# Performance work log

Measured on AMD Instinct MI355X. Metric: run time of the kernel, lower is better.

Reference implementation:

```python
import jax, jax.numpy as jnp
import numpy as np

SCORE_THRESH = 0.5
NMS_THRESH = 0.4
TOP_K = 1000  # fixed pre-NMS candidate budget (jit-safe replacement for boolean masking)
STRIDES = (8, 16, 32)
H, W = 2176, 3840


def _anchor_centers(fh, fw, stride):
    yv, xv = jnp.meshgrid(jnp.arange(fh), jnp.arange(fw), indexing='ij')
    return (jnp.stack([xv, yv], -1).reshape(-1, 2).astype(jnp.float32)) * stride  # [N,2]


def _decode_level(scores, bbox, kps, stride):
    fh, fw = H // stride, W // stride
    c = _anchor_centers(fh, fw, stride)                 # [N,2]
    s = jax.nn.sigmoid(scores.reshape(-1))              # [N]
    d = bbox.reshape(-1, 4) * stride                    # [N,4]
    boxes = jnp.concatenate([c - d[:, :2], c + d[:, 2:4]], axis=1)  # x1y1x2y2
    k = kps.reshape(-1, 5, 2) * stride + c[:, None, :]  # (x,y) pairs
    return s, boxes, k.reshape(-1, 10)


def _iou_matrix(b):
    area = (b[:, 2] - b[:, 0]) * (b[:, 3] - b[:, 1])
    lt = jnp.maximum(b[:, None, :2], b[None, :, :2])
    rb = jnp.minimum(b[:, None, 2:], b[None, :, 2:])
    wh = jnp.clip(rb - lt, 0.0)
    inter = wh[..., 0] * wh[..., 1]
    return inter / jnp.clip(area[:, None] + area[None, :] - inter, 1e-9)


def _nms_keep(iou, valid):
    n = iou.shape[0]
    ar = jnp.arange(n)

    def body(i, keep):
        sup = (iou[i] > NMS_THRESH) & (ar > i) & keep[i]
        return keep & ~sup

    return jax.lax.fori_loop(0, n, body, valid)


def reference(x, scores8, bbox8, kps8, scores16, bbox16, kps16, scores32, bbox32, kps32):
    levels = ((scores8, bbox8, kps8), (scores16, bbox16, kps16), (scores32, bbox32, kps32))
    ss, bs, ks = [], [], []
    for (s, b, k), stride in zip(levels, STRIDES):
        si, bi, ki = _decode_level(s, b, k, stride)
        ss.append(si); bs.append(bi); ks.append(ki)
    scores = jnp.concatenate(ss)   # [N_total]
    boxes = jnp.concatenate(bs)    # [N_total,4]
    kpss = jnp.concatenate(ks)     # [N_total,10]

    masked = jnp.where(scores > SCORE_THRESH, scores, -1.0)
    top_s, idx = jax.lax.top_k(masked, TOP_K)
    valid = top_s > SCORE_THRESH
    b = boxes[idx]
    k = kpss[idx]

    keep = jax.lax.stop_gradient(_nms_keep(_iou_matrix(b), valid))
    final_boxes = jnp.where(keep[:, None], b, 0.0)
    final_scores = jnp.where(keep, top_s, 0.0)
    final_kpss = jnp.where(keep[:, None], k, 0.0)
    return final_boxes, final_scores, final_kpss


def setup_inputs() -> dict:
    key = jax.random.key(0)
    ks = jax.random.split(key, 10)
    n8 = (H // 8) * (W // 8)
    n16 = (H // 16) * (W // 16)
    n32 = (H // 32) * (W // 32)
    return {
        'x': jax.random.normal(ks[0], (1, 3, H, W), jnp.float32),
        'scores8': jax.random.normal(ks[1], (1, n8, 1), jnp.float32),
        'bbox8': jax.random.uniform(ks[2], (1, n8, 4), jnp.float32),
        'kps8': jax.random.normal(ks[3], (1, n8, 10), jnp.float32),
        'scores16': jax.random.normal(ks[4], (1, n16, 1), jnp.float32),
        'bbox16': jax.random.uniform(ks[5], (1, n16, 4), jnp.float32),
        'kps16': jax.random.normal(ks[6], (1, n16, 10), jnp.float32),
        'scores32': jax.random.normal(ks[7], (1, n32, 1), jnp.float32),
        'bbox32': jax.random.uniform(ks[8], (1, n32, 4), jnp.float32),
        'kps32': jax.random.normal(ks[9], (1, n32, 10), jnp.float32),
    }
```

## Files before the change

kernel.cpp:

```cpp
#include <hip/hip_runtime.h>
#include <stdint.h>

typedef unsigned int u32;
typedef unsigned long long u64;

#define N8   130560
#define N16  32640
#define N32  8160
#define NTOT 171360
#define NTOT4 42840
#define TOPK 1000
#define NWORDS 16
#define NBINS 512
#define BUCKET_SCALE 85.25f
#define LIST_CAP 2016
#define CPB 32
#define HIST_BLKS 84
#define HIST_THR 512
#define CMP_BLKS 168
#define RANK_BLKS 63
#define IOU_BLKS 63
#define IOU_TASKS (TOPK * NWORDS)
#define NMS_CACHE 256


#define MI_CNT 0
#define MI_IOU 128
#define META_U32 256

#define OFF_PART 0
#define OFF_META 86016
#define OFF_NZ   87040
#define OFF_LIST 87168
#define OFF_MASK 103296

__device__ __forceinline__ u64 ald64(const u64* p) {
  return __hip_atomic_load(p, __ATOMIC_RELAXED, __HIP_MEMORY_SCOPE_AGENT);
}
__device__ __forceinline__ void ast64(u64* p, u64 v) {
  __hip_atomic_store(p, v, __ATOMIC_RELAXED, __HIP_MEMORY_SCOPE_AGENT);
}

__device__ __forceinline__ u32 bucket_of(float x) {
  u32 b = (u32)(x * BUCKET_SCALE);
  return b > (NBINS - 1) ? (NBINS - 1) : b;
}

__device__ __forceinline__ float4 load_logit4(int v, const float* s8, const float* s16,
                                              const float* s32) {
  int e = v * 4;
  if (e < N8) return ((const float4*)s8)[v];
  if (e < N8 + N16) return ((const float4*)s16)[v - N8 / 4];
  return ((const float4*)s32)[v - (N8 + N16) / 4];
}

__device__ __forceinline__ bool iou_gt04(float4 a, float4 b) {
#pragma clang fp contract(off)
  float areaA = (a.z - a.x) * (a.w - a.y);
  float areaB = (b.z - b.x) * (b.w - b.y);
  float ltx = fmaxf(a.x, b.x);
  float lty = fmaxf(a.y, b.y);
  float rbx = fminf(a.z, b.z);
  float rby = fminf(a.w, b.w);
  float wx = rbx - ltx; wx = wx > 0.0f ? wx : 0.0f;
  float wy = rby - lty; wy = wy > 0.0f ? wy : 0.0f;
  float inter = wx * wy;
  float un = areaA + areaB - inter;
  un = un > 1e-9f ? un : 1e-9f;
  return (inter / un) > 0.4f;
}

__device__ __forceinline__ u64 valid_word(int w, u32 vcnt) {
  int lo = w * 64;
  if ((int)vcnt >= lo + 64) return ~0ull;
  if ((int)vcnt <= lo) return 0ull;
  return (1ull << (vcnt - (u32)lo)) - 1ull;
}

__global__ void __launch_bounds__(HIST_THR) k1_hist(
    const float* __restrict__ s8, const float* __restrict__ s16, const float* __restrict__ s32,
    u32* __restrict__ part, u32* __restrict__ meta, u64* __restrict__ nz) {
  __shared__ u32 lh[NBINS];
  const int t = threadIdx.x, blk = blockIdx.x;
  if (t < NBINS) lh[t] = 0;
  __syncthreads();
  int v = blk * HIST_THR + t;
  if (v < NTOT4) {
    float4 x = load_logit4(v, s8, s16, s32);
    if (x.x > 0.0f) atomicAdd(&lh[bucket_of(x.x)], 1u);
    if (x.y > 0.0f) atomicAdd(&lh[bucket_of(x.y)], 1u);
    if (x.z > 0.0f) atomicAdd(&lh[bucket_of(x.z)], 1u);
    if (x.w > 0.0f) atomicAdd(&lh[bucket_of(x.w)], 1u);
  }
  __syncthreads();
  if (t < 256)
    part[blk * 256 + t] = lh[2 * t] | (lh[2 * t + 1] << 16);
  if (blk == 0) {
    if (t < META_U32) meta[t] = 0;
    if (t < NWORDS) nz[t] = 0ull;
  }
}

__global__ void __launch_bounds__(256) k4_compact(
    const float* __restrict__ s8, const float* __restrict__ s16, const float* __restrict__ s32,
    const u32* __restrict__ part, u32* __restrict__ meta, u64* __restrict__ list) {
  __shared__ u32 csum[256];
  __shared__ u32 sB, sBase;
  __shared__ u32 cnt16[16];
  const int t = threadIdx.x, blk = blockIdx.x;
  const int wave = t >> 6, lane = t & 63;
  const int v = blk * 256 + t;
  float4 x = make_float4(-1.f, -1.f, -1.f, -1.f);
  if (v < NTOT4) x = load_logit4(v, s8, s16, s32);

  u32 lo = 0, hi = 0;
  {
    int p = 0;
    for (; p + 4 <= HIST_BLKS; p += 4) {
      u32 a0 = part[(p + 0) * 256 + t];
      u32 a1 = part[(p + 1) * 256 + t];
      u32 a2 = part[(p + 2) * 256 + t];
      u32 a3 = part[(p + 3) * 256 + t];
      lo += (a0 & 0xFFFFu) + (a1 & 0xFFFFu) + (a2 & 0xFFFFu) + (a3 & 0xFFFFu);
      hi += (a0 >> 16) + (a1 >> 16) + (a2 >> 16) + (a3 >> 16);
    }
    for (; p < HIST_BLKS; ++p) {
      u32 a = part[p * 256 + t];
      lo += a & 0xFFFFu; hi += a >> 16;
    }
  }
  csum[t] = lo + hi;
  __syncthreads();
  for (int off = 1; off < 256; off <<= 1) {
    u32 add = (t + off < 256) ? csum[t + off] : 0u;
    __syncthreads();
    csum[t] += add;
    __syncthreads();
  }
  u32 above = (t < 255) ? csum[t + 1] : 0u;
  if (t == 0 && csum[0] < TOPK) sB = 0u;
  if (csum[t] >= TOPK && above < TOPK)
    sB = (above + hi >= TOPK) ? (u32)(2 * t + 1) : (u32)(2 * t);
  __syncthreads();

  const u32 B = sB;
  float c[4] = {x.x, x.y, x.z, x.w};
  u32 win = 0;
#pragma unroll
  for (int j = 0; j < 4; ++j)
    if (c[j] > 0.0f && bucket_of(c[j]) >= B) win |= 1u << j;
  u32 wpos[4], wcnt[4];
#pragma unroll
  for (int j = 0; j < 4; ++j) {
    u64 bal = __ballot((win >> j) & 1u);
    wcnt[j] = (u32)__popcll(bal);
    wpos[j] = (u32)__popcll(bal & ((1ull << lane) - 1ull));
  }
  if (lane == 0) {
#pragma unroll
    for (int j = 0; j < 4; ++j) cnt16[wave * 4 + j] = wcnt[j];
  }
  __syncthreads();
  if (t == 0) {
    u32 tot = 0, pre[16];
#pragma unroll
    for (int k = 0; k < 16; ++k) { pre[k] = tot; tot += cnt16[k]; }
#pragma unroll
    for (int k = 0; k < 16; ++k) cnt16[k] = pre[k];
    sBase = tot ? atomicAdd(&meta[MI_CNT], tot) : 0u;
  }
  __syncthreads();
#pragma unroll
  for (int j = 0; j < 4; ++j) {
    if ((win >> j) & 1u) {
      u32 dst = sBase + cnt16[wave * 4 + j] + wpos[j];
      if (dst < LIST_CAP) {
        u32 idx = (u32)(v * 4 + j);
        list[dst] = ((u64)__float_as_uint(c[j]) << 32) | (u64)(~idx);
      }
    }
  }
}

__global__ void __launch_bounds__(256) k5_rank(
    const u32* __restrict__ meta, const u64* __restrict__ list,
    const float* __restrict__ bb8,  const float* __restrict__ kp8,
    const float* __restrict__ bb16, const float* __restrict__ kp16,
    const float* __restrict__ bb32, const float* __restrict__ kp32,
    float* __restrict__ out) {
  __shared__ __align__(16) u64 keys[LIST_CAP];
  __shared__ u32 rpart[256];
  __shared__ u32 sCnt;
  const int t = threadIdx.x, blk = blockIdx.x;
  if (t == 0) { u32 cc = meta[MI_CNT]; sCnt = cc > LIST_CAP ? LIST_CAP : cc; }
  __syncthreads();
  const u32 cnt = sCnt;
  for (int j = t; j < LIST_CAP; j += 256) keys[j] = (j < (int)cnt) ? list[j] : 0ull;
  __syncthreads();
  {
    const int ci = t & 31, sl = t >> 5;
    const int c = blk * CPB + ci;
    const int chunk = ((int)cnt + 7) >> 3;
    int lo = sl * chunk; if (lo > (int)cnt) lo = (int)cnt;
    int hi = lo + chunk; if (hi > (int)cnt) hi = (int)cnt;
    u64 my = keys[c];
    int r = 0, j = lo;
    for (; j + 4 <= hi; j += 4)
      r += (keys[j] > my) + (keys[j + 1] > my) + (keys[j + 2] > my) + (keys[j + 3] > my);
    for (; j < hi; ++j) r += (keys[j] > my);
    rpart[t] = (u32)r;
  }
  __syncthreads();
  if (t < CPB) {
    const int c = blk * CPB + t;
    if (c < (int)cnt) {
      int rank = 0;
#pragma unroll
      for (int q = 0; q < 8; ++q) rank += (int)rpart[t + 32 * q];
      if (rank < TOPK) {
        u64 my = keys[c];
        float lx = __uint_as_float((u32)(my >> 32));
        float sc = (float)(1.0 / (1.0 + exp(-(double)lx)));
        u32 idx = ~((u32)my);
        float4 box;
        float kv[10];
        int p, xq, yq;
        float st;
        const float *bb, *kp;
        if (idx < N8) {
          st = 8.f;  p = (int)idx;              xq = p % 480; yq = p / 480; bb = bb8;  kp = kp8;
        } else if (idx < N8 + N16) {
          st = 16.f; p = (int)idx - N8;         xq = p % 240; yq = p / 240; bb = bb16; kp = kp16;
        } else {
          st = 32.f; p = (int)idx - (N8 + N16); xq = p % 120; yq = p / 120; bb = bb32; kp = kp32;
        }
        float cx = (float)xq * st, cy = (float)yq * st;
        {
#pragma clang fp contract(off)
          float d0 = bb[4 * p + 0] * st;
          float d1 = bb[4 * p + 1] * st;
          float d2 = bb[4 * p + 2] * st;
          float d3 = bb[4 * p + 3] * st;
          box.x = cx - d0; box.y = cy - d1; box.z = cx + d2; box.w = cy + d3;
          for (int q = 0; q < 10; ++q)
            kv[q] = kp[10 * p + q] * st + ((q & 1) ? cy : cx);
        }
        ((float4*)out)[rank] = box;
        out[4000 + rank] = sc;
#pragma unroll
        for (int q = 0; q < 10; ++q) out[5000 + 10 * rank + q] = kv[q];
      }
    } else if (c < TOPK) {
      ((float4*)out)[c] = make_float4(0.f, 0.f, 0.f, 0.f);
      out[4000 + c] = 0.f;
#pragma unroll
      for (int q = 0; q < 10; ++q) out[5000 + 10 * c + q] = 0.f;
    }
  }
}

__global__ void __launch_bounds__(256) k67_iou_nms(
    u32* meta, u64* nzWords, u64* mask, float* out) {
  __shared__ __align__(16) char smem[36864];
  __shared__ int isLast;
  __shared__ u32 sPc[16], sOff17[17];
  __shared__ u64 sRem[NWORDS];
  const int t = threadIdx.x, blk = blockIdx.x;

  float4* boxes = (float4*)smem;
  for (int r = t; r < TOPK; r += 256) boxes[r] = ((const float4*)out)[r];
  __syncthreads();
  int task = blk * 256 + t;
  if (task < IOU_TASKS) {
    int w = task / 1000;
    int i = task - w * 1000;
    float4 a = boxes[i];
    int bse = w * 64;
    int jend = (bse + 64) < TOPK ? (bse + 64) : TOPK;
    u64 bits = 0;
    for (int j = bse; j < jend; ++j)
      if (j > i && iou_gt04(a, boxes[j])) bits |= 1ull << (j - bse);
    ast64(&mask[(u64)w * 1000 + i], bits);
    if (bits) atomicOr(&nzWords[i >> 6], 1ull << (i & 63));
  }
  __syncthreads();
  if (t == 0)
    isLast = (__hip_atomic_fetch_add(&meta[MI_IOU], 1u, __ATOMIC_RELAXED,
                                     __HIP_MEMORY_SCOPE_AGENT) == (u32)(IOU_BLKS - 1));
  __syncthreads();
  if (!isLast) return;

  u32 cc = meta[MI_CNT];
  if (cc > LIST_CAP) cc = LIST_CAP;
  const u32 vcnt = cc < TOPK ? cc : TOPK;
  u32* rows = (u32*)smem;
  u64* cache = (u64*)(smem + 4096);
  u64 nzv = 0;
  if (t < NWORDS) {
    nzv = ald64(&nzWords[t]) & valid_word(t, vcnt);
    sPc[t] = (u32)__popcll(nzv);
  }
  __syncthreads();
  if (t == 0) {
    u32 o = 0;
    for (int w = 0; w < NWORDS; ++w) { sOff17[w] = o; o += sPc[w]; }
    sOff17[16] = o;
  }
  __syncthreads();
  if (t < NWORDS) {
    u64 m = nzv;
    u32 o = sOff17[t];
    while (m) { int b = __builtin_ctzll(m); m &= m - 1; rows[o++] = (u32)(t * 64 + b); }
  }
  __syncthreads();
  const int S = (int)sOff17[16];
  const int Sc = S < NMS_CACHE ? S : NMS_CACHE;
  for (int idx = t; idx < Sc * NWORDS; idx += 256) {
    int s = idx >> 4, w = idx & 15;
    cache[s * NWORDS + w] = ald64(&mask[(u64)w * 1000 + rows[s]]);
  }
  __syncthreads();
  if (t < 64) {
    u64 remv = 0;
    for (int s = 0; s < S; ++s) {
      u32 row = rows[s];
      int c = (int)(row >> 6), b = (int)(row & 63);
      u64 remc = __shfl(remv, c);
      if (!((remc >> b) & 1ull)) {
        u64 m = 0;
        if (t < NWORDS)
          m = (s < NMS_CACHE) ? cache[s * NWORDS + t] : ald64(&mask[(u64)t * 1000 + row]);
        remv |= m;
      }
    }
    if (t < NWORDS) sRem[t] = valid_word(t, vcnt) & remv;
  }
  __syncthreads();
  for (int r = t; r < TOPK; r += 256) {
    if ((sRem[r >> 6] >> (r & 63)) & 1ull) {
      ((float4*)out)[r] = make_float4(0.f, 0.f, 0.f, 0.f);
      out[4000 + r] = 0.f;
#pragma unroll
      for (int q = 0; q < 10; ++q) out[5000 + 10 * r + q] = 0.f;
    }
  }
}

extern "C" void kernel_launch(void* const* d_in, const int* in_sizes, int n_in,
                              void* d_out, int out_size, void* d_ws, size_t ws_size,
                              hipStream_t stream) {
  const float* s8   = (const float*)d_in[1];
  const float* bb8  = (const float*)d_in[2];
  const float* kp8  = (const float*)d_in[3];
  const float* s16  = (const float*)d_in[4];
  const float* bb16 = (const float*)d_in[5];
  const float* kp16 = (const float*)d_in[6];
  const float* s32  = (const float*)d_in[7];
  const float* bb32 = (const float*)d_in[8];
  const float* kp32 = (const float*)d_in[9];

  char* ws = (char*)d_ws;
  u32* part    = (u32*)(ws + OFF_PART);
  u32* meta    = (u32*)(ws + OFF_META);
  u64* nzWords = (u64*)(ws + OFF_NZ);
  u64* list    = (u64*)(ws + OFF_LIST);
  u64* mask    = (u64*)(ws + OFF_MASK);
  float* out   = (float*)d_out;

  k1_hist<<<HIST_BLKS, HIST_THR, 0, stream>>>(s8, s16, s32, part, meta, nzWords);
  k4_compact<<<CMP_BLKS, 256, 0, stream>>>(s8, s16, s32, part, meta, list);
  k5_rank<<<RANK_BLKS, 256, 0, stream>>>(meta, list, bb8, kp8, bb16, kp16, bb32, kp32, out);
  k67_iou_nms<<<IOU_BLKS, 256, 0, stream>>>(meta, nzWords, mask, out);
}
```

Before: 166.7 us.

## Fuse rank, IoU mask and NMS into one kernel via compact-order boxes

Box decoding moves into the compaction kernel, which writes each candidate's box into a compact-order buffer. The rank kernel then builds IoU suppression bitmasks in compact-list order, comparing score keys instead of waiting for ranked outputs, and the last block runs the greedy NMS sweep through a rank-to-compact index map. This removes one kernel launch and the dependency on boxes being written in rank order. In exchange the mask doubles to 32 words over up to 2016 entries, the rank kernel does more per-block IoU work, and the NMS cache shrinks.

```diff
diff --git a/kernel.cpp b/kernel.cpp
--- a/kernel.cpp
+++ b/kernel.cpp
@@ -11,6 +11,7 @@
 #define NTOT4 42840
 #define TOPK 1000
 #define NWORDS 16
+#define CWORDS 32
 #define NBINS 512
 #define BUCKET_SCALE 85.25f
 #define LIST_CAP 2016
@@ -18,24 +19,30 @@
 #define HIST_BLKS 84
 #define HIST_THR 512
 #define CMP_BLKS 168
-#define RANK_BLKS 63
-#define IOU_BLKS 63
-#define IOU_TASKS (TOPK * NWORDS)
-#define NMS_CACHE 256
+#define K5_BLKS 63
+#define NMS_CACHE 192
 
 
 #define MI_CNT 0
-#define MI_IOU 128
+#define MI_K5  128
 #define META_U32 256
 
 #define OFF_PART 0
 #define OFF_META 86016
 #define OFF_NZ   87040
 #define OFF_LIST 87168
-#define OFF_MASK 103296
-
+#define OFF_CBOX 103296
+#define OFF_R2C  135552
+#define OFF_MASK 139552
+
+__device__ __forceinline__ u32 ald32(const u32* p) {
+  return __hip_atomic_load(p, __ATOMIC_RELAXED, __HIP_MEMORY_SCOPE_AGENT);
+}
 __device__ __forceinline__ u64 ald64(const u64* p) {
   return __hip_atomic_load(p, __ATOMIC_RELAXED, __HIP_MEMORY_SCOPE_AGENT);
+}
+__device__ __forceinline__ void ast32(u32* p, u32 v) {
+  __hip_atomic_store(p, v, __ATOMIC_RELAXED, __HIP_MEMORY_SCOPE_AGENT);
 }
 __device__ __forceinline__ void ast64(u64* p, u64 v) {
   __hip_atomic_store(p, v, __ATOMIC_RELAXED, __HIP_MEMORY_SCOPE_AGENT);
@@ -77,6 +84,17 @@
   return (1ull << (vcnt - (u32)lo)) - 1ull;
 }
 
+__device__ __forceinline__ void level_of(u32 idx, int& p, int& xq, int& yq, float& st,
+                                         int& lvl) {
+  if (idx < N8) {
+    st = 8.f;  p = (int)idx;              xq = p % 480; yq = p / 480; lvl = 0;
+  } else if (idx < N8 + N16) {
+    st = 16.f; p = (int)idx - N8;         xq = p % 240; yq = p / 240; lvl = 1;
+  } else {
+    st = 32.f; p = (int)idx - (N8 + N16); xq = p % 120; yq = p / 120; lvl = 2;
+  }
+}
+
 __global__ void __launch_bounds__(HIST_THR) k1_hist(
     const float* __restrict__ s8, const float* __restrict__ s16, const float* __restrict__ s32,
     u32* __restrict__ part, u32* __restrict__ meta, u64* __restrict__ nz) {
@@ -103,7 +121,9 @@
 
 __global__ void __launch_bounds__(256) k4_compact(
     const float* __restrict__ s8, const float* __restrict__ s16, const float* __restrict__ s32,
-    const u32* __restrict__ part, u32* __restrict__ meta, u64* __restrict__ list) {
+    const float* __restrict__ bb8, const float* __restrict__ bb16, const float* __restrict__ bb32,
+    const u32* __restrict__ part, u32* __restrict__ meta, u64* __restrict__ list,
+    float4* __restrict__ cbox) {
   __shared__ u32 csum[256];
   __shared__ u32 sB, sBase;
   __shared__ u32 cnt16[16];
@@ -177,26 +197,52 @@
       if (dst < LIST_CAP) {
         u32 idx = (u32)(v * 4 + j);
         list[dst] = ((u64)__float_as_uint(c[j]) << 32) | (u64)(~idx);
+        int p, xq, yq, lvl;
+        float st;
+        level_of(idx, p, xq, yq, st, lvl);
+        const float* bb = (lvl == 0) ? bb8 : (lvl == 1) ? bb16 : bb32;
+        float4 d = ((const float4*)bb)[p];
+        float cx = (float)xq * st, cy = (float)yq * st;
+        float4 box;
+        {
+#pragma clang fp contract(off)
+          box.x = cx - d.x * st; box.y = cy - d.y * st;
+          box.z = cx + d.z * st; box.w = cy + d.w * st;
+        }
+        cbox[dst] = box;
       }
     }
   }
 }
 
-__global__ void __launch_bounds__(256) k5_rank(
-    const u32* __restrict__ meta, const u64* __restrict__ list,
-    const float* __restrict__ bb8,  const float* __restrict__ kp8,
-    const float* __restrict__ bb16, const float* __restrict__ kp16,
-    const float* __restrict__ bb32, const float* __restrict__ kp32,
-    float* __restrict__ out) {
-  __shared__ __align__(16) u64 keys[LIST_CAP];
+__global__ void __launch_bounds__(256) k5_all(
+    u32* meta, const u64* __restrict__ list, const float4* __restrict__ cbox_g,
+    const float* __restrict__ kp8, const float* __restrict__ kp16,
+    const float* __restrict__ kp32,
+    u64* nzr, u64* mask, u32* r2c_g, float* out) {
+  __shared__ __align__(16) char smem[57344];
   __shared__ u32 rpart[256];
+  __shared__ u32 rankOf[CPB];
+  __shared__ u64 rownz[CPB * 8];
   __shared__ u32 sCnt;
+  __shared__ int isLast;
+  __shared__ u32 sPc[NWORDS], sOff17[NWORDS + 1];
+  __shared__ u64 sRem32[CWORDS];
   const int t = threadIdx.x, blk = blockIdx.x;
+  u64* o64 = (u64*)out;
+
+  u64* keys = (u64*)smem;
+  float4* cbox = (float4*)(smem + 16384);
+
   if (t == 0) { u32 cc = meta[MI_CNT]; sCnt = cc > LIST_CAP ? LIST_CAP : cc; }
   __syncthreads();
   const u32 cnt = sCnt;
-  for (int j = t; j < LIST_CAP; j += 256) keys[j] = (j < (int)cnt) ? list[j] : 0ull;
-  __syncthreads();
+  for (int j = t; j < LIST_CAP; j += 256) {
+    keys[j] = (j < (int)cnt) ? list[j] : 0ull;
+    cbox[j] = (j < (int)cnt) ? cbox_g[j] : make_float4(0.f, 0.f, 0.f, 0.f);
+  }
+  __syncthreads();
+
   {
     const int ci = t & 31, sl = t >> 5;
     const int c = blk * CPB + ci;
@@ -211,100 +257,110 @@
     rpart[t] = (u32)r;
   }
   __syncthreads();
+
   if (t < CPB) {
     const int c = blk * CPB + t;
+    u32 rk = 0xFFFFFFFFu;
     if (c < (int)cnt) {
       int rank = 0;
 #pragma unroll
       for (int q = 0; q < 8; ++q) rank += (int)rpart[t + 32 * q];
       if (rank < TOPK) {
+        rk = (u32)rank;
         u64 my = keys[c];
         float lx = __uint_as_float((u32)(my >> 32));
         float sc = (float)(1.0 / (1.0 + exp(-(double)lx)));
         u32 idx = ~((u32)my);
-        float4 box;
+        int p, xq, yq, lvl;
+        float st;
+        level_of(idx, p, xq, yq, st, lvl);
+        const float* kp = (lvl == 0) ? kp8 : (lvl == 1) ? kp16 : kp32;
+        float cx = (float)xq * st, cy = (float)yq * st;
         float kv[10];
-        int p, xq, yq;
-        float st;
-        const float *bb, *kp;
-        if (idx < N8) {
-          st = 8.f;  p = (int)idx;              xq = p % 480; yq = p / 480; bb = bb8;  kp = kp8;
-        } else if (idx < N8 + N16) {
-          st = 16.f; p = (int)idx - N8;         xq = p % 240; yq = p / 240; bb = bb16; kp = kp16;
-        } else {
-          st = 32.f; p = (int)idx - (N8 + N16); xq = p % 120; yq = p / 120; bb = bb32; kp = kp32;
-        }
-        float cx = (float)xq * st, cy = (float)yq * st;
         {
 #pragma clang fp contract(off)
-          float d0 = bb[4 * p + 0] * st;
-          float d1 = bb[4 * p + 1] * st;
-          float d2 = bb[4 * p + 2] * st;
-          float d3 = bb[4 * p + 3] * st;
-          box.x = cx - d0; box.y = cy - d1; box.z = cx + d2; box.w = cy + d3;
           for (int q = 0; q < 10; ++q)
             kv[q] = kp[10 * p + q] * st + ((q & 1) ? cy : cx);
         }
-        ((float4*)out)[rank] = box;
-        out[4000 + rank] = sc;
-#pragma unroll
-        for (int q = 0; q < 10; ++q) out[5000 + 10 * rank + q] = kv[q];
+        float4 box = cbox[c];
+        ast64(&o64[2 * rank],     ((u64)__float_as_uint(box.y) << 32) | __float_as_uint(box.x));
+        ast64(&o64[2 * rank + 1], ((u64)__float_as_uint(box.w) << 32) | __float_as_uint(box.z));
+        ast32(&((u32*)out)[4000 + rank], __float_as_uint(sc));
+        int wb = 2500 + 5 * rank;
+#pragma unroll
+        for (int q = 0; q < 5; ++q)
+          ast64(&o64[wb + q],
+                ((u64)__float_as_uint(kv[2 * q + 1]) << 32) | __float_as_uint(kv[2 * q]));
+        ast32(&r2c_g[rank], (u32)c);
       }
     } else if (c < TOPK) {
-      ((float4*)out)[c] = make_float4(0.f, 0.f, 0.f, 0.f);
-      out[4000 + c] = 0.f;
-#pragma unroll
-      for (int q = 0; q < 10; ++q) out[5000 + 10 * c + q] = 0.f;
-    }
-  }
-}
-
-__global__ void __launch_bounds__(256) k67_iou_nms(
-    u32* meta, u64* nzWords, u64* mask, float* out) {
-  __shared__ __align__(16) char smem[36864];
-  __shared__ int isLast;
-  __shared__ u32 sPc[16], sOff17[17];
-  __shared__ u64 sRem[NWORDS];
-  const int t = threadIdx.x, blk = blockIdx.x;
-
-  float4* boxes = (float4*)smem;
-  for (int r = t; r < TOPK; r += 256) boxes[r] = ((const float4*)out)[r];
-  __syncthreads();
-  int task = blk * 256 + t;
-  if (task < IOU_TASKS) {
-    int w = task / 1000;
-    int i = task - w * 1000;
-    float4 a = boxes[i];
-    int bse = w * 64;
-    int jend = (bse + 64) < TOPK ? (bse + 64) : TOPK;
-    u64 bits = 0;
-    for (int j = bse; j < jend; ++j)
-      if (j > i && iou_gt04(a, boxes[j])) bits |= 1ull << (j - bse);
-    ast64(&mask[(u64)w * 1000 + i], bits);
-    if (bits) atomicOr(&nzWords[i >> 6], 1ull << (i & 63));
+      ast64(&o64[2 * c], 0ull); ast64(&o64[2 * c + 1], 0ull);
+      ast32(&((u32*)out)[4000 + c], 0u);
+      int wb = 2500 + 5 * c;
+#pragma unroll
+      for (int q = 0; q < 5; ++q) ast64(&o64[wb + q], 0ull);
+    }
+    rankOf[t] = rk;
+  }
+  __syncthreads();
+
+  {
+    const int ci = t & 31, sl = t >> 5;
+    const u32 r = rankOf[ci];
+    u64 w0 = 0, w1 = 0, w2 = 0, w3 = 0;
+    if (r != 0xFFFFFFFFu) {
+      const int c = blk * CPB + ci;
+      const u64 myKey = keys[c];
+      const float4 a = cbox[c];
+      const int j0 = sl * 256;
+      const int jend = (j0 + 256 < LIST_CAP) ? 256 : (LIST_CAP - j0);
+      for (int jj = 0; jj < jend; ++jj) {
+        const int j = j0 + jj;
+        if (keys[j] < myKey && iou_gt04(a, cbox[j])) {
+          u64 bit = 1ull << (jj & 63);
+          if (jj < 64) w0 |= bit; else if (jj < 128) w1 |= bit;
+          else if (jj < 192) w2 |= bit; else w3 |= bit;
+        }
+      }
+      const int wbase = sl * 4;
+      ast64(&mask[(u64)(wbase + 0) * 1000 + r], w0);
+      ast64(&mask[(u64)(wbase + 1) * 1000 + r], w1);
+      ast64(&mask[(u64)(wbase + 2) * 1000 + r], w2);
+      ast64(&mask[(u64)(wbase + 3) * 1000 + r], w3);
+    }
+    rownz[ci * 8 + sl] = w0 | w1 | w2 | w3;
+  }
+  __syncthreads();
+  if (t < CPB) {
+    const u32 r = rankOf[t];
+    u64 nzrow = rownz[t * 8 + 0] | rownz[t * 8 + 1] | rownz[t * 8 + 2] | rownz[t * 8 + 3]
+              | rownz[t * 8 + 4] | rownz[t * 8 + 5] | rownz[t * 8 + 6] | rownz[t * 8 + 7];
+    if (r != 0xFFFFFFFFu && nzrow)
+      atomicOr(&nzr[r >> 6], 1ull << (r & 63));
   }
   __syncthreads();
   if (t == 0)
-    isLast = (__hip_atomic_fetch_add(&meta[MI_IOU], 1u, __ATOMIC_RELAXED,
-                                     __HIP_MEMORY_SCOPE_AGENT) == (u32)(IOU_BLKS - 1));
+    isLast = (__hip_atomic_fetch_add(&meta[MI_K5], 1u, __ATOMIC_RELAXED,
+                                     __HIP_MEMORY_SCOPE_AGENT) == (u32)(K5_BLKS - 1));
   __syncthreads();
   if (!isLast) return;
 
-  u32 cc = meta[MI_CNT];
-  if (cc > LIST_CAP) cc = LIST_CAP;
-  const u32 vcnt = cc < TOPK ? cc : TOPK;
+  const u32 vcnt = cnt < TOPK ? cnt : TOPK;
   u32* rows = (u32*)smem;
-  u64* cache = (u64*)(smem + 4096);
+  u32* r2cL = (u32*)(smem + 4096);
+  u64* cache = (u64*)(smem + 8192);
   u64 nzv = 0;
   if (t < NWORDS) {
-    nzv = ald64(&nzWords[t]) & valid_word(t, vcnt);
+    nzv = ald64(&nzr[t]) & valid_word(t, vcnt);
     sPc[t] = (u32)__popcll(nzv);
   }
+  for (int r = t; r < TOPK; r += 256)
+    r2cL[r] = (r < (int)vcnt) ? ald32(&r2c_g[r]) : 0u;
   __syncthreads();
   if (t == 0) {
     u32 o = 0;
     for (int w = 0; w < NWORDS; ++w) { sOff17[w] = o; o += sPc[w]; }
-    sOff17[16] = o;
+    sOff17[NWORDS] = o;
   }
   __syncthreads();
   if (t < NWORDS) {
@@ -313,35 +369,40 @@
     while (m) { int b = __builtin_ctzll(m); m &= m - 1; rows[o++] = (u32)(t * 64 + b); }
   }
   __syncthreads();
-  const int S = (int)sOff17[16];
+  const int S = (int)sOff17[NWORDS];
   const int Sc = S < NMS_CACHE ? S : NMS_CACHE;
-  for (int idx = t; idx < Sc * NWORDS; idx += 256) {
-    int s = idx >> 4, w = idx & 15;
-    cache[s * NWORDS + w] = ald64(&mask[(u64)w * 1000 + rows[s]]);
+  for (int idx = t; idx < Sc * CWORDS; idx += 256) {
+    int s = idx >> 5, w = idx & 31;
+    cache[s * CWORDS + w] = ald64(&mask[(u64)w * 1000 + rows[s]]);
   }
   __syncthreads();
   if (t < 64) {
     u64 remv = 0;
     for (int s = 0; s < S; ++s) {
-      u32 row = rows[s];
-      int c = (int)(row >> 6), b = (int)(row & 63);
-      u64 remc = __shfl(remv, c);
-      if (!((remc >> b) & 1ull)) {
+      u32 r = rows[s];
+      u32 c = r2cL[r];
+      int cl = (int)(c >> 6), cb = (int)(c & 63);
+      u64 remc = __shfl(remv, cl);
+      if (!((remc >> cb) & 1ull)) {
         u64 m = 0;
-        if (t < NWORDS)
-          m = (s < NMS_CACHE) ? cache[s * NWORDS + t] : ald64(&mask[(u64)t * 1000 + row]);
+        if (t < CWORDS)
+          m = (s < NMS_CACHE) ? cache[s * CWORDS + t] : ald64(&mask[(u64)t * 1000 + r]);
         remv |= m;
       }
     }
-    if (t < NWORDS) sRem[t] = valid_word(t, vcnt) & remv;
+    if (t < CWORDS) sRem32[t] = remv;
   }
   __syncthreads();
   for (int r = t; r < TOPK; r += 256) {
-    if ((sRem[r >> 6] >> (r & 63)) & 1ull) {
-      ((float4*)out)[r] = make_float4(0.f, 0.f, 0.f, 0.f);
-      out[4000 + r] = 0.f;
-#pragma unroll
-      for (int q = 0; q < 10; ++q) out[5000 + 10 * r + q] = 0.f;
+    if (r < (int)vcnt) {
+      u32 c = r2cL[r];
+      if ((sRem32[c >> 6] >> (c & 63)) & 1ull) {
+        ast64(&o64[2 * r], 0ull); ast64(&o64[2 * r + 1], 0ull);
+        ast32(&((u32*)out)[4000 + r], 0u);
+        int wb = 2500 + 5 * r;
+#pragma unroll
+        for (int q = 0; q < 5; ++q) ast64(&o64[wb + q], 0ull);
+      }
     }
   }
 }
@@ -362,13 +423,16 @@
   char* ws = (char*)d_ws;
   u32* part    = (u32*)(ws + OFF_PART);
   u32* meta    = (u32*)(ws + OFF_META);
-  u64* nzWords = (u64*)(ws + OFF_NZ);
+  u64* nzr     = (u64*)(ws + OFF_NZ);
   u64* list    = (u64*)(ws + OFF_LIST);
+  float4* cbox = (float4*)(ws + OFF_CBOX);
+  u32* r2c     = (u32*)(ws + OFF_R2C);
   u64* mask    = (u64*)(ws + OFF_MASK);
   float* out   = (float*)d_out;
 
-  k1_hist<<<HIST_BLKS, HIST_THR, 0, stream>>>(s8, s16, s32, part, meta, nzWords);
-  k4_compact<<<CMP_BLKS, 256, 0, stream>>>(s8, s16, s32, part, meta, list);
-  k5_rank<<<RANK_BLKS, 256, 0, stream>>>(meta, list, bb8, kp8, bb16, kp16, bb32, kp32, out);
-  k67_iou_nms<<<IOU_BLKS, 256, 0, stream>>>(meta, nzWords, mask, out);
-}
+  k1_hist<<<HIST_BLKS, HIST_THR, 0, stream>>>(s8, s16, s32, part, meta, nzr);
+  k4_compact<<<CMP_BLKS, 256, 0, stream>>>(s8, s16, s32, bb8, bb16, bb32,
+                                           part, meta, list, cbox);
+  k5_all<<<K5_BLKS, 256, 0, stream>>>(meta, list, cbox, kp8, kp16, kp32,
+                                      nzr, mask, r2c, out);
+}
```

Result: slower. 208.0 us (+24.8%).
